# Kernel optimization log

Measured on AMD Instinct MI355X. Metric: run time of the kernel, lower is better.

The kernel has to match this reference:

```python
import jax, jax.numpy as jnp
import numpy as np

B, N_VEC, N_DIM, N_W, N_HID, VOCAB, N_CLASS = 16, 2048, 32, 4, 128, 32000, 10


def setup_inputs() -> dict:
    key = jax.random.key(0)
    ks = jax.random.split(key, 8)
    data = jax.random.randint(ks[0], (B, N_VEC), 0, VOCAB, dtype=jnp.int64)
    emb = jax.random.normal(ks[1], (VOCAB, N_DIM), dtype=jnp.float32) * 0.1
    # stacked per-layer weights for the n_W WModules: Linear(n_dim->n_hid), GELU, Linear(n_hid->n_vec)
    fw1 = jax.random.normal(ks[2], (N_W, N_DIM, N_HID), dtype=jnp.float32) * (1.0 / np.sqrt(N_DIM))
    fb1 = jnp.zeros((N_W, N_HID), dtype=jnp.float32)
    fw2 = jax.random.normal(ks[3], (N_W, N_HID, N_VEC), dtype=jnp.float32) * (1.0 / np.sqrt(N_HID))
    fb2 = jnp.zeros((N_W, N_VEC), dtype=jnp.float32)
    Wf = jax.random.normal(ks[4], (N_VEC * N_DIM, N_CLASS), dtype=jnp.float32) * (1.0 / np.sqrt(N_VEC * N_DIM))
    bf = jnp.zeros((N_CLASS,), dtype=jnp.float32)
    return {"data": data, "emb": emb, "fw1": fw1, "fb1": fb1, "fw2": fw2, "fb2": fb2, "Wf": Wf, "bf": bf}


def reference(data, emb, fw1, fb1, fw2, fb2, Wf, bf):
    X = emb[data]                       # [B, n_vec, n_dim]
    V = X                               # g is identity (with_g=False)
    # iterate over self.fs[::-1]: indices n_W-1 .. 0
    for i in range(N_W - 1, -1, -1):
        h = jax.nn.gelu(jnp.einsum('bnd,dh->bnh', X, fw1[i]) + fb1[i], approximate=False)
        W = jnp.einsum('bnh,hm->bnm', h, fw2[i]) + fb2[i]   # [B, n_vec, n_vec]
        V = jnp.einsum('bnm,bmd->bnd', W, V)                # [B, n_vec, n_dim]
    out = V.reshape(V.shape[0], -1) @ Wf + bf               # [B, n_class]
    return out
```

## Files before the change

kernel.cpp:

```cpp
#include <hip/hip_runtime.h>

#define NB 16
#define NVEC 2048
#define NDIM 32
#define NW 4
#define NHID 128
#define NCLASS 10
#define MS 16
#define USIZE (129 * 32)

__device__ __forceinline__ float gelu_fast(float x) {
    float t = 1.5957691216057308f * x * (1.0f + 0.044715f * x * x);
    return x / (1.0f + __expf(-t));
}

__global__ __launch_bounds__(256) void k_embed(const int* __restrict__ data,
                                               const float* __restrict__ emb,
                                               const float* __restrict__ bf,
                                               float* __restrict__ X,
                                               float* __restrict__ out) {
    int gid = blockIdx.x * 256 + threadIdx.x;
    int row = gid >> 3, sub = gid & 7;
    ((float4*)X)[gid] = ((const float4*)emb)[data[row] * 8 + sub];
    if (blockIdx.x == 0 && threadIdx.x < NB * NCLASS)
        out[threadIdx.x] = bf[threadIdx.x % NCLASS];
}

__global__ __launch_bounds__(1024) void k_U(const float* __restrict__ V,
                                            const float* __restrict__ fw2,
                                            const float* __restrict__ fb2,
                                            float* __restrict__ Upart) {
    __shared__ float Vs[128 * 32];
    __shared__ float cred[4][33];
    int ms = blockIdx.x, b = blockIdx.y;
    int tid = threadIdx.x;
    int m0 = ms * 128;
    ((float4*)Vs)[tid] = ((const float4*)(V + (b * NVEC + m0) * NDIM))[tid];
    int k1 = tid & 127, d0 = (tid >> 7) * 4;
    const float* wrow = fw2 + k1 * NVEC + m0;
    float acc[4] = {0.f, 0.f, 0.f, 0.f};
    __syncthreads();
#pragma unroll
    for (int mt = 0; mt < 128; mt += 16) {
        float4 w4[4];
#pragma unroll
        for (int j = 0; j < 4; ++j) w4[j] = ((const float4*)(wrow + mt))[j];
        const float* wf = (const float*)w4;
#pragma unroll
        for (int j = 0; j < 16; ++j) {
            float w = wf[j];
            float4 v = *(const float4*)&Vs[(mt + j) * 32 + d0];
            acc[0] += w * v.x; acc[1] += w * v.y;
            acc[2] += w * v.z; acc[3] += w * v.w;
        }
    }
    float* Up = Upart + ((size_t)ms * NB + b) * USIZE;
    *(float4*)&Up[k1 * 32 + d0] = make_float4(acc[0], acc[1], acc[2], acc[3]);
    if (tid < 128) {
        int d = tid & 31, seg = tid >> 5;
        float ca = 0.f;
#pragma unroll 8
        for (int mm = seg * 32; mm < seg * 32 + 32; ++mm)
            ca += fb2[m0 + mm] * Vs[mm * 32 + d];
        cred[seg][d] = ca;
    }
    __syncthreads();
    if (tid < 32)
        Up[128 * 32 + tid] = cred[0][tid] + cred[1][tid] + cred[2][tid] + cred[3][tid];
}

__global__ __launch_bounds__(256) void k_Ured(const float* __restrict__ Upart,
                                              float* __restrict__ U) {
    int b = blockIdx.x;
    int i4 = blockIdx.y * 129 + threadIdx.x;
    if (threadIdx.x >= 129) return;
    float4 s = ((const float4*)Upart)[(size_t)b * (USIZE / 4) + i4];
#pragma unroll
    for (int ms = 1; ms < MS; ++ms) {
        float4 v = ((const float4*)Upart)[((size_t)ms * NB + b) * (USIZE / 4) + i4];
        s.x += v.x; s.y += v.y; s.z += v.z; s.w += v.w;
    }
    ((float4*)U)[b * (USIZE / 4) + i4] = s;
}

template <bool LAST>
__global__ __launch_bounds__(256) void k_applyF(const float* __restrict__ X,
                                                const float* __restrict__ fw1l,
                                                const float* __restrict__ fb1l,
                                                const float* __restrict__ U,
                                                float* __restrict__ Vout,
                                                const float* __restrict__ Wf,
                                                float* __restrict__ out) {
    __shared__ float Us[USIZE];
    __shared__ float w1s[NDIM * NHID];
    __shared__ float xs[64][33];
    __shared__ float hs[64 * 132];
    __shared__ float ored[4][NCLASS];
    int ng = blockIdx.x, b = blockIdx.y;
    int tid = threadIdx.x;
    int n0 = ng * 64;

    for (int i4 = tid; i4 < USIZE / 4; i4 += 256)
        ((float4*)Us)[i4] = ((const float4*)(U + (size_t)b * USIZE))[i4];
#pragma unroll
    for (int j = 0; j < 4; ++j)
        ((float4*)w1s)[tid + j * 256] = ((const float4*)fw1l)[tid + j * 256];
#pragma unroll
    for (int j = 0; j < 2; ++j) {
        int i4 = tid + j * 256;
        float4 v = ((const float4*)(X + (b * NVEC + n0) * NDIM))[i4];
        int r = i4 >> 3, c4 = (i4 & 7) * 4;
        xs[r][c4] = v.x; xs[r][c4 + 1] = v.y;
        xs[r][c4 + 2] = v.z; xs[r][c4 + 3] = v.w;
    }
    __syncthreads();

    {
        int kg = tid & 15, rg = tid >> 4;
        int k0 = kg * 8, r0 = rg * 4;
        float acc[4][8];
#pragma unroll
        for (int j = 0; j < 8; ++j) {
            float bv = fb1l[k0 + j];
            acc[0][j] = bv; acc[1][j] = bv; acc[2][j] = bv; acc[3][j] = bv;
        }
#pragma unroll 8
        for (int d = 0; d < NDIM; ++d) {
            float4 wa = *(const float4*)&w1s[d * NHID + k0];
            float4 wb = *(const float4*)&w1s[d * NHID + k0 + 4];
            float wk[8] = {wa.x, wa.y, wa.z, wa.w, wb.x, wb.y, wb.z, wb.w};
            float x0 = xs[r0][d], x1 = xs[r0 + 1][d];
            float x2 = xs[r0 + 2][d], x3 = xs[r0 + 3][d];
#pragma unroll
            for (int j = 0; j < 8; ++j) {
                acc[0][j] += x0 * wk[j];
                acc[1][j] += x1 * wk[j];
                acc[2][j] += x2 * wk[j];
                acc[3][j] += x3 * wk[j];
            }
        }
#pragma unroll
        for (int r = 0; r < 4; ++r) {
            float4 o0, o1;
            o0.x = gelu_fast(acc[r][0]); o0.y = gelu_fast(acc[r][1]);
            o0.z = gelu_fast(acc[r][2]); o0.w = gelu_fast(acc[r][3]);
            o1.x = gelu_fast(acc[r][4]); o1.y = gelu_fast(acc[r][5]);
            o1.z = gelu_fast(acc[r][6]); o1.w = gelu_fast(acc[r][7]);
            *(float4*)&hs[(r0 + r) * 132 + k0] = o0;
            *(float4*)&hs[(r0 + r) * 132 + k0 + 4] = o1;
        }
    }
    __syncthreads();

    {
        int dg = tid & 7, rga = tid >> 3;
        int d0 = dg * 4, r0 = rga * 2;
        float4 a0 = *(const float4*)&Us[NHID * 32 + d0];
        float4 a1 = a0;
#pragma unroll 8
        for (int k = 0; k < NHID; k += 4) {
            float4 h0 = *(const float4*)&hs[r0 * 132 + k];
            float4 h1 = *(const float4*)&hs[(r0 + 1) * 132 + k];
            float4 u0 = *(const float4*)&Us[(k + 0) * 32 + d0];
            float4 u1 = *(const float4*)&Us[(k + 1) * 32 + d0];
            float4 u2 = *(const float4*)&Us[(k + 2) * 32 + d0];
            float4 u3 = *(const float4*)&Us[(k + 3) * 32 + d0];
            a0.x += h0.x * u0.x + h0.y * u1.x + h0.z * u2.x + h0.w * u3.x;
            a0.y += h0.x * u0.y + h0.y * u1.y + h0.z * u2.y + h0.w * u3.y;
            a0.z += h0.x * u0.z + h0.y * u1.z + h0.z * u2.z + h0.w * u3.z;
            a0.w += h0.x * u0.w + h0.y * u1.w + h0.z * u2.w + h0.w * u3.w;
            a1.x += h1.x * u0.x + h1.y * u1.x + h1.z * u2.x + h1.w * u3.x;
            a1.y += h1.x * u0.y + h1.y * u1.y + h1.z * u2.y + h1.w * u3.y;
            a1.z += h1.x * u0.z + h1.y * u1.z + h1.z * u2.z + h1.w * u3.z;
            a1.w += h1.x * u0.w + h1.y * u1.w + h1.z * u2.w + h1.w * u3.w;
        }
        if constexpr (!LAST) {
            *(float4*)&Vout[(b * NVEC + n0 + r0) * NDIM + d0] = a0;
            *(float4*)&Vout[(b * NVEC + n0 + r0 + 1) * NDIM + d0] = a1;
        } else {
            float accC[NCLASS];
#pragma unroll
            for (int c = 0; c < NCLASS; ++c) accC[c] = 0.f;
            float va[2][4] = {{a0.x, a0.y, a0.z, a0.w}, {a1.x, a1.y, a1.z, a1.w}};
#pragma unroll
            for (int r = 0; r < 2; ++r)
#pragma unroll
                for (int dd = 0; dd < 4; ++dd) {
                    int jj = (n0 + r0 + r) * NDIM + d0 + dd;
                    const float2* wr = (const float2*)(Wf + (size_t)jj * NCLASS);
                    float v = va[r][dd];
#pragma unroll
                    for (int p = 0; p < 5; ++p) {
                        float2 w = wr[p];
                        accC[2 * p]     += v * w.x;
                        accC[2 * p + 1] += v * w.y;
                    }
                }
            int lane = tid & 63, wv = tid >> 6;
#pragma unroll
            for (int c = 0; c < NCLASS; ++c)
#pragma unroll
                for (int off = 32; off >= 1; off >>= 1)
                    accC[c] += __shfl_down(accC[c], off, 64);
            if (lane == 0) {
#pragma unroll
                for (int c = 0; c < NCLASS; ++c) ored[wv][c] = accC[c];
            }
            __syncthreads();
            if (tid < NCLASS)
                atomicAdd(&out[b * NCLASS + tid],
                          ored[0][tid] + ored[1][tid] + ored[2][tid] + ored[3][tid]);
        }
    }
}

extern "C" void kernel_launch(void* const* d_in, const int* in_sizes, int n_in,
                              void* d_out, int out_size, void* d_ws, size_t ws_size,
                              hipStream_t stream) {
    const int*   data = (const int*)d_in[0];
    const float* emb  = (const float*)d_in[1];
    const float* fw1  = (const float*)d_in[2];
    const float* fb1  = (const float*)d_in[3];
    const float* fw2  = (const float*)d_in[4];
    const float* fb2  = (const float*)d_in[5];
    const float* Wf   = (const float*)d_in[6];
    const float* bf   = (const float*)d_in[7];
    float* out = (float*)d_out;

    float* X     = (float*)d_ws;
    float* VA    = X + NB * NVEC * NDIM;
    float* VB    = VA + NB * NVEC * NDIM;
    float* Upart = VB + NB * NVEC * NDIM;
    float* U     = Upart + (size_t)MS * NB * USIZE;

    k_embed<<<dim3(NB * NVEC * NDIM / 4 / 256), 256, 0, stream>>>(data, emb, bf, X, out);

    const float* Vcur = X;
    float* Vnext = VA;
    for (int t = 0; t < NW; ++t) {
        int i = NW - 1 - t;
        k_U<<<dim3(MS, NB), 1024, 0, stream>>>(Vcur, fw2 + (size_t)i * NHID * NVEC,
                                               fb2 + (size_t)i * NVEC, Upart);
        k_Ured<<<dim3(NB, 8), 256, 0, stream>>>(Upart, U);
        if (i > 0) {
            k_applyF<false><<<dim3(NVEC / 64, NB), 256, 0, stream>>>(
                X, fw1 + (size_t)i * NDIM * NHID, fb1 + (size_t)i * NHID,
                U, Vnext, nullptr, nullptr);
            Vcur = Vnext;
            Vnext = (Vnext == VA) ? VB : VA;
        } else {
            k_applyF<true><<<dim3(NVEC / 64, NB), 256, 0, stream>>>(
                X, fw1, fb1, U, nullptr, Wf, out);
        }
    }
}
```

Baseline: 219.6 us.

## Restructure U and applyF kernels around register-resident weight tiles

k_U now runs 256 threads per block. Each thread keeps 64 fw2 weights and 32 accumulators in registers and reads V rows straight from global memory with broadcast loads instead of staging them in LDS. The fb2 bias term moves into an extra block row of k_Ured. k_applyF now handles 128 rows per block: w1 sits in registers, U is read directly from global, the hidden dimension is split across wave pairs and reduced through LDS, and each wave issues its classifier atomics directly. The aim is less LDS traffic and more reuse per thread, at the cost of heavy register pressure and fewer blocks.

```diff
diff --git a/kernel.cpp b/kernel.cpp
--- a/kernel.cpp
+++ b/kernel.cpp
@@ -8,6 +8,7 @@
 #define NCLASS 10
 #define MS 16
 #define USIZE (129 * 32)
+#define UPSZ  (128 * 32)
 
 __device__ __forceinline__ float gelu_fast(float x) {
     float t = 1.5957691216057308f * x * (1.0f + 0.044715f * x * x);
@@ -26,61 +27,94 @@
         out[threadIdx.x] = bf[threadIdx.x % NCLASS];
 }
 
-__global__ __launch_bounds__(1024) void k_U(const float* __restrict__ V,
-                                            const float* __restrict__ fw2,
-                                            const float* __restrict__ fb2,
-                                            float* __restrict__ Upart) {
-    __shared__ float Vs[128 * 32];
-    __shared__ float cred[4][33];
+__global__ __launch_bounds__(256) void k_U(const float* __restrict__ V,
+                                           const float* __restrict__ fw2,
+                                           float* __restrict__ Upart) {
+    __shared__ float part[2][64 * 32];
     int ms = blockIdx.x, b = blockIdx.y;
+    int tid = threadIdx.x, lane = tid & 63;
+    int wv = __builtin_amdgcn_readfirstlane(tid >> 6);
+    int kh = wv & 1, mh = wv >> 1;
+    int k = kh * 64 + lane;
+    int m0 = ms * 128 + mh * 64;
+
+    float wreg[64];
+    {
+        const float4* wr = (const float4*)(fw2 + (size_t)k * NVEC + m0);
+#pragma unroll
+        for (int j = 0; j < 16; ++j) {
+            float4 v = wr[j];
+            wreg[4 * j] = v.x; wreg[4 * j + 1] = v.y;
+            wreg[4 * j + 2] = v.z; wreg[4 * j + 3] = v.w;
+        }
+    }
+    float acc[32];
+#pragma unroll
+    for (int d = 0; d < 32; ++d) acc[d] = 0.f;
+
+    const float4* Vr = (const float4*)(V + ((size_t)b * NVEC + m0) * NDIM);
+#pragma unroll 2
+    for (int mm = 0; mm < 64; ++mm) {
+        float w = wreg[mm];
+        float4 vv[8];
+#pragma unroll
+        for (int j = 0; j < 8; ++j) vv[j] = Vr[mm * 8 + j];
+#pragma unroll
+        for (int j = 0; j < 8; ++j) {
+            acc[4 * j + 0] += w * vv[j].x;
+            acc[4 * j + 1] += w * vv[j].y;
+            acc[4 * j + 2] += w * vv[j].z;
+            acc[4 * j + 3] += w * vv[j].w;
+        }
+    }
+    if (mh == 1) {
+#pragma unroll
+        for (int d = 0; d < 32; ++d) part[kh][d * 64 + lane] = acc[d];
+    }
+    __syncthreads();
+    if (mh == 0) {
+#pragma unroll
+        for (int d = 0; d < 32; ++d) acc[d] += part[kh][d * 64 + lane];
+        float* Up = Upart + ((size_t)ms * NB + b) * UPSZ;
+#pragma unroll
+        for (int j = 0; j < 8; ++j)
+            *(float4*)&Up[k * 32 + j * 4] =
+                make_float4(acc[4 * j], acc[4 * j + 1], acc[4 * j + 2], acc[4 * j + 3]);
+    }
+}
+
+__global__ __launch_bounds__(256) void k_Ured(const float* __restrict__ Upart,
+                                              const float* __restrict__ V,
+                                              const float* __restrict__ fb2,
+                                              float* __restrict__ U) {
+    int b = blockIdx.x, y = blockIdx.y;
     int tid = threadIdx.x;
-    int m0 = ms * 128;
-    ((float4*)Vs)[tid] = ((const float4*)(V + (b * NVEC + m0) * NDIM))[tid];
-    int k1 = tid & 127, d0 = (tid >> 7) * 4;
-    const float* wrow = fw2 + k1 * NVEC + m0;
-    float acc[4] = {0.f, 0.f, 0.f, 0.f};
-    __syncthreads();
-#pragma unroll
-    for (int mt = 0; mt < 128; mt += 16) {
-        float4 w4[4];
-#pragma unroll
-        for (int j = 0; j < 4; ++j) w4[j] = ((const float4*)(wrow + mt))[j];
-        const float* wf = (const float*)w4;
-#pragma unroll
-        for (int j = 0; j < 16; ++j) {
-            float w = wf[j];
-            float4 v = *(const float4*)&Vs[(mt + j) * 32 + d0];
-            acc[0] += w * v.x; acc[1] += w * v.y;
-            acc[2] += w * v.z; acc[3] += w * v.w;
-        }
-    }
-    float* Up = Upart + ((size_t)ms * NB + b) * USIZE;
-    *(float4*)&Up[k1 * 32 + d0] = make_float4(acc[0], acc[1], acc[2], acc[3]);
-    if (tid < 128) {
+    if (y < 8) {
+        if (tid < 128) {
+            int i4 = y * 128 + tid;
+            float4 s = ((const float4*)(Upart + (size_t)b * UPSZ))[i4];
+#pragma unroll
+            for (int ms = 1; ms < MS; ++ms) {
+                float4 v = ((const float4*)(Upart + ((size_t)ms * NB + b) * UPSZ))[i4];
+                s.x += v.x; s.y += v.y; s.z += v.z; s.w += v.w;
+            }
+            ((float4*)(U + (size_t)b * USIZE))[i4] = s;
+        }
+    } else {
+        __shared__ float red[8][33];
         int d = tid & 31, seg = tid >> 5;
         float ca = 0.f;
-#pragma unroll 8
-        for (int mm = seg * 32; mm < seg * 32 + 32; ++mm)
-            ca += fb2[m0 + mm] * Vs[mm * 32 + d];
-        cred[seg][d] = ca;
-    }
-    __syncthreads();
-    if (tid < 32)
-        Up[128 * 32 + tid] = cred[0][tid] + cred[1][tid] + cred[2][tid] + cred[3][tid];
-}
-
-__global__ __launch_bounds__(256) void k_Ured(const float* __restrict__ Upart,
-                                              float* __restrict__ U) {
-    int b = blockIdx.x;
-    int i4 = blockIdx.y * 129 + threadIdx.x;
-    if (threadIdx.x >= 129) return;
-    float4 s = ((const float4*)Upart)[(size_t)b * (USIZE / 4) + i4];
-#pragma unroll
-    for (int ms = 1; ms < MS; ++ms) {
-        float4 v = ((const float4*)Upart)[((size_t)ms * NB + b) * (USIZE / 4) + i4];
-        s.x += v.x; s.y += v.y; s.z += v.z; s.w += v.w;
-    }
-    ((float4*)U)[b * (USIZE / 4) + i4] = s;
+        for (int m = seg * 256; m < seg * 256 + 256; ++m)
+            ca += fb2[m] * V[((size_t)b * NVEC + m) * NDIM + d];
+        red[seg][d] = ca;
+        __syncthreads();
+        if (tid < 32) {
+            float s = 0.f;
+#pragma unroll
+            for (int j = 0; j < 8; ++j) s += red[j][tid];
+            U[(size_t)b * USIZE + 128 * 32 + tid] = s;
+        }
+    }
 }
 
 template <bool LAST>
@@ -91,112 +125,100 @@
                                                 float* __restrict__ Vout,
                                                 const float* __restrict__ Wf,
                                                 float* __restrict__ out) {
-    __shared__ float Us[USIZE];
-    __shared__ float w1s[NDIM * NHID];
-    __shared__ float xs[64][33];
-    __shared__ float hs[64 * 132];
-    __shared__ float ored[4][NCLASS];
+    __shared__ float hsm[128 * 129];
     int ng = blockIdx.x, b = blockIdx.y;
-    int tid = threadIdx.x;
-    int n0 = ng * 64;
-
-    for (int i4 = tid; i4 < USIZE / 4; i4 += 256)
-        ((float4*)Us)[i4] = ((const float4*)(U + (size_t)b * USIZE))[i4];
-#pragma unroll
-    for (int j = 0; j < 4; ++j)
-        ((float4*)w1s)[tid + j * 256] = ((const float4*)fw1l)[tid + j * 256];
-#pragma unroll
-    for (int j = 0; j < 2; ++j) {
-        int i4 = tid + j * 256;
-        float4 v = ((const float4*)(X + (b * NVEC + n0) * NDIM))[i4];
-        int r = i4 >> 3, c4 = (i4 & 7) * 4;
-        xs[r][c4] = v.x; xs[r][c4 + 1] = v.y;
-        xs[r][c4 + 2] = v.z; xs[r][c4 + 3] = v.w;
-    }
-    __syncthreads();
-
-    {
-        int kg = tid & 15, rg = tid >> 4;
-        int k0 = kg * 8, r0 = rg * 4;
-        float acc[4][8];
-#pragma unroll
-        for (int j = 0; j < 8; ++j) {
-            float bv = fb1l[k0 + j];
-            acc[0][j] = bv; acc[1][j] = bv; acc[2][j] = bv; acc[3][j] = bv;
-        }
-#pragma unroll 8
-        for (int d = 0; d < NDIM; ++d) {
-            float4 wa = *(const float4*)&w1s[d * NHID + k0];
-            float4 wb = *(const float4*)&w1s[d * NHID + k0 + 4];
-            float wk[8] = {wa.x, wa.y, wa.z, wa.w, wb.x, wb.y, wb.z, wb.w};
-            float x0 = xs[r0][d], x1 = xs[r0 + 1][d];
-            float x2 = xs[r0 + 2][d], x3 = xs[r0 + 3][d];
-#pragma unroll
-            for (int j = 0; j < 8; ++j) {
-                acc[0][j] += x0 * wk[j];
-                acc[1][j] += x1 * wk[j];
-                acc[2][j] += x2 * wk[j];
-                acc[3][j] += x3 * wk[j];
-            }
-        }
-#pragma unroll
-        for (int r = 0; r < 4; ++r) {
-            float4 o0, o1;
-            o0.x = gelu_fast(acc[r][0]); o0.y = gelu_fast(acc[r][1]);
-            o0.z = gelu_fast(acc[r][2]); o0.w = gelu_fast(acc[r][3]);
-            o1.x = gelu_fast(acc[r][4]); o1.y = gelu_fast(acc[r][5]);
-            o1.z = gelu_fast(acc[r][6]); o1.w = gelu_fast(acc[r][7]);
-            *(float4*)&hs[(r0 + r) * 132 + k0] = o0;
-            *(float4*)&hs[(r0 + r) * 132 + k0 + 4] = o1;
-        }
-    }
-    __syncthreads();
-
-    {
-        int dg = tid & 7, rga = tid >> 3;
-        int d0 = dg * 4, r0 = rga * 2;
-        float4 a0 = *(const float4*)&Us[NHID * 32 + d0];
-        float4 a1 = a0;
-#pragma unroll 8
-        for (int k = 0; k < NHID; k += 4) {
-            float4 h0 = *(const float4*)&hs[r0 * 132 + k];
-            float4 h1 = *(const float4*)&hs[(r0 + 1) * 132 + k];
-            float4 u0 = *(const float4*)&Us[(k + 0) * 32 + d0];
-            float4 u1 = *(const float4*)&Us[(k + 1) * 32 + d0];
-            float4 u2 = *(const float4*)&Us[(k + 2) * 32 + d0];
-            float4 u3 = *(const float4*)&Us[(k + 3) * 32 + d0];
-            a0.x += h0.x * u0.x + h0.y * u1.x + h0.z * u2.x + h0.w * u3.x;
-            a0.y += h0.x * u0.y + h0.y * u1.y + h0.z * u2.y + h0.w * u3.y;
-            a0.z += h0.x * u0.z + h0.y * u1.z + h0.z * u2.z + h0.w * u3.z;
-            a0.w += h0.x * u0.w + h0.y * u1.w + h0.z * u2.w + h0.w * u3.w;
-            a1.x += h1.x * u0.x + h1.y * u1.x + h1.z * u2.x + h1.w * u3.x;
-            a1.y += h1.x * u0.y + h1.y * u1.y + h1.z * u2.y + h1.w * u3.y;
-            a1.z += h1.x * u0.z + h1.y * u1.z + h1.z * u2.z + h1.w * u3.z;
-            a1.w += h1.x * u0.w + h1.y * u1.w + h1.z * u2.w + h1.w * u3.w;
+    int tid = threadIdx.x, lane = tid & 63;
+    int wv = __builtin_amdgcn_readfirstlane(tid >> 6);
+    int rg = wv >> 1, kh = wv & 1;
+    int n0 = ng * 128;
+    int kf = kh * 64 + lane;
+
+    float w1reg[32];
+#pragma unroll
+    for (int d = 0; d < 32; ++d) w1reg[d] = fw1l[d * NHID + kf];
+    float b1 = fb1l[kf];
+
+    const float* Xb = X + ((size_t)b * NVEC + n0 + rg * 64) * NDIM;
+    for (int rr = 0; rr < 64; rr += 2) {
+        const float4* x0 = (const float4*)(Xb + rr * 32);
+        const float4* x1 = (const float4*)(Xb + rr * 32 + 32);
+        float a0 = b1, a0b = 0.f, a1 = b1, a1b = 0.f;
+#pragma unroll
+        for (int j = 0; j < 8; ++j) {
+            float4 v0 = x0[j], v1 = x1[j];
+            a0  += v0.x * w1reg[4 * j + 0];
+            a0b += v0.y * w1reg[4 * j + 1];
+            a0  += v0.z * w1reg[4 * j + 2];
+            a0b += v0.w * w1reg[4 * j + 3];
+            a1  += v1.x * w1reg[4 * j + 0];
+            a1b += v1.y * w1reg[4 * j + 1];
+            a1  += v1.z * w1reg[4 * j + 2];
+            a1b += v1.w * w1reg[4 * j + 3];
+        }
+        int r = rg * 64 + rr;
+        hsm[r * 129 + kf]       = gelu_fast(a0 + a0b);
+        hsm[(r + 1) * 129 + kf] = gelu_fast(a1 + a1b);
+    }
+    __syncthreads();
+
+    float oacc[32];
+#pragma unroll
+    for (int d = 0; d < 32; ++d) oacc[d] = 0.f;
+    int rowA = rg * 64 + lane;
+    const float* hrow = &hsm[rowA * 129 + kh * 64];
+    const float4* Ub4 = (const float4*)(U + (size_t)b * USIZE) + (size_t)kh * 64 * 8;
+#pragma unroll 2
+    for (int kk = 0; kk < 64; ++kk) {
+        float hv = hrow[kk];
+        float4 uu[8];
+#pragma unroll
+        for (int j = 0; j < 8; ++j) uu[j] = Ub4[kk * 8 + j];
+#pragma unroll
+        for (int j = 0; j < 8; ++j) {
+            oacc[4 * j + 0] += hv * uu[j].x;
+            oacc[4 * j + 1] += hv * uu[j].y;
+            oacc[4 * j + 2] += hv * uu[j].z;
+            oacc[4 * j + 3] += hv * uu[j].w;
+        }
+    }
+    __syncthreads();
+    if (kh == 1) {
+#pragma unroll
+        for (int d = 0; d < 32; ++d) hsm[rowA * 33 + d] = oacc[d];
+    }
+    __syncthreads();
+    if (kh == 0) {
+        const float4* Ubias = (const float4*)(U + (size_t)b * USIZE + 128 * 32);
+#pragma unroll
+        for (int j = 0; j < 8; ++j) {
+            float4 ub = Ubias[j];
+            oacc[4 * j + 0] += hsm[rowA * 33 + 4 * j + 0] + ub.x;
+            oacc[4 * j + 1] += hsm[rowA * 33 + 4 * j + 1] + ub.y;
+            oacc[4 * j + 2] += hsm[rowA * 33 + 4 * j + 2] + ub.z;
+            oacc[4 * j + 3] += hsm[rowA * 33 + 4 * j + 3] + ub.w;
         }
         if constexpr (!LAST) {
-            *(float4*)&Vout[(b * NVEC + n0 + r0) * NDIM + d0] = a0;
-            *(float4*)&Vout[(b * NVEC + n0 + r0 + 1) * NDIM + d0] = a1;
+            float* vo = Vout + ((size_t)b * NVEC + n0 + rowA) * NDIM;
+#pragma unroll
+            for (int j = 0; j < 8; ++j)
+                *(float4*)&vo[j * 4] = make_float4(oacc[4 * j], oacc[4 * j + 1],
+                                                   oacc[4 * j + 2], oacc[4 * j + 3]);
         } else {
             float accC[NCLASS];
 #pragma unroll
             for (int c = 0; c < NCLASS; ++c) accC[c] = 0.f;
-            float va[2][4] = {{a0.x, a0.y, a0.z, a0.w}, {a1.x, a1.y, a1.z, a1.w}};
-#pragma unroll
-            for (int r = 0; r < 2; ++r)
-#pragma unroll
-                for (int dd = 0; dd < 4; ++dd) {
-                    int jj = (n0 + r0 + r) * NDIM + d0 + dd;
-                    const float2* wr = (const float2*)(Wf + (size_t)jj * NCLASS);
-                    float v = va[r][dd];
-#pragma unroll
-                    for (int p = 0; p < 5; ++p) {
-                        float2 w = wr[p];
-                        accC[2 * p]     += v * w.x;
-                        accC[2 * p + 1] += v * w.y;
-                    }
+            int nrow = n0 + rowA;
+#pragma unroll
+            for (int d = 0; d < 32; ++d) {
+                float v = oacc[d];
+                const float2* wr = (const float2*)(Wf + ((size_t)nrow * 32 + d) * NCLASS);
+#pragma unroll
+                for (int p = 0; p < 5; ++p) {
+                    float2 w = wr[p];
+                    accC[2 * p]     += v * w.x;
+                    accC[2 * p + 1] += v * w.y;
                 }
-            int lane = tid & 63, wv = tid >> 6;
+            }
 #pragma unroll
             for (int c = 0; c < NCLASS; ++c)
 #pragma unroll
@@ -204,12 +226,9 @@
                     accC[c] += __shfl_down(accC[c], off, 64);
             if (lane == 0) {
 #pragma unroll
-                for (int c = 0; c < NCLASS; ++c) ored[wv][c] = accC[c];
+                for (int c = 0; c < NCLASS; ++c)
+                    atomicAdd(&out[b * NCLASS + c], accC[c]);
             }
-            __syncthreads();
-            if (tid < NCLASS)
-                atomicAdd(&out[b * NCLASS + tid],
-                          ored[0][tid] + ored[1][tid] + ored[2][tid] + ored[3][tid]);
         }
     }
 }
@@ -231,7 +250,7 @@
     float* VA    = X + NB * NVEC * NDIM;
     float* VB    = VA + NB * NVEC * NDIM;
     float* Upart = VB + NB * NVEC * NDIM;
-    float* U     = Upart + (size_t)MS * NB * USIZE;
+    float* U     = Upart + (size_t)MS * NB * UPSZ;
 
     k_embed<<<dim3(NB * NVEC * NDIM / 4 / 256), 256, 0, stream>>>(data, emb, bf, X, out);
 
@@ -239,17 +258,16 @@
     float* Vnext = VA;
     for (int t = 0; t < NW; ++t) {
         int i = NW - 1 - t;
-        k_U<<<dim3(MS, NB), 1024, 0, stream>>>(Vcur, fw2 + (size_t)i * NHID * NVEC,
-                                               fb2 + (size_t)i * NVEC, Upart);
-        k_Ured<<<dim3(NB, 8), 256, 0, stream>>>(Upart, U);
+        k_U<<<dim3(MS, NB), 256, 0, stream>>>(Vcur, fw2 + (size_t)i * NHID * NVEC, Upart);
+        k_Ured<<<dim3(NB, 9), 256, 0, stream>>>(Upart, Vcur, fb2 + (size_t)i * NVEC, U);
         if (i > 0) {
-            k_applyF<false><<<dim3(NVEC / 64, NB), 256, 0, stream>>>(
+            k_applyF<false><<<dim3(NVEC / 128, NB), 256, 0, stream>>>(
                 X, fw1 + (size_t)i * NDIM * NHID, fb1 + (size_t)i * NHID,
                 U, Vnext, nullptr, nullptr);
             Vcur = Vnext;
             Vnext = (Vnext == VA) ? VB : VA;
         } else {
-            k_applyF<true><<<dim3(NVEC / 64, NB), 256, 0, stream>>>(
+            k_applyF<true><<<dim3(NVEC / 128, NB), 256, 0, stream>>>(
                 X, fw1, fb1, U, nullptr, Wf, out);
         }
     }
```

Result: slower. 341.2 us (+55.4%).
